# Optimization experiments

Hardware: AMD Instinct MI355X
Metric: run time of the kernel (lower is better)

Reference implementation:

```python
import jax, jax.numpy as jnp
import numpy as np

V, N, K, D = 2, 100000, 8, 128
TAU = 1.0
LOG_2PI = float(np.log(2.0 * np.pi))


def setup_inputs() -> dict:
    key = jax.random.key(0)
    k1, k2, k3 = jax.random.split(key, 3)
    z = jax.random.normal(k1, (V, N, D), dtype=jnp.float32)
    phi = jnp.ones((V, K), dtype=jnp.float32) / K
    mu = jax.random.normal(k2, (V, K, D), dtype=jnp.float32)
    # sigma: identity (as in torch init) plus a small symmetric PSD perturbation
    a = 0.05 * jax.random.normal(k3, (V, K, D, D), dtype=jnp.float32)
    sigma = jnp.eye(D, dtype=jnp.float32) + jnp.einsum('vkde,vkfe->vkdf', a, a)
    return {"z": z, "phi": phi, "mu": mu, "sigma": sigma}


def _compute_energy(z, phi, mu, sigma):
    # z: [N, D]; phi: [K]; mu: [K, D]; sigma: [K, D, D]
    eps_eye = 1e-6 * jnp.eye(D, dtype=z.dtype)
    sigma_stable = sigma + eps_eye  # [K, D, D]
    inv_sigma = jnp.linalg.inv(sigma_stable)
    det_sigma = jnp.clip(jnp.linalg.det(sigma_stable), 1e-6, None)  # [K]
    diff = z[:, None, :] - mu[None, :, :]  # [N, K, D]
    maha = jnp.einsum('nkd,kde,nke->nk', diff, inv_sigma, diff)  # [N, K]
    log_pi = jax.nn.log_softmax(phi)  # [K]
    log_prob = (-0.5 * maha
                - 0.5 * D * LOG_2PI
                - 0.5 * jnp.log(det_sigma)[None, :]
                + log_pi[None, :])  # [N, K]
    energy = -jax.nn.logsumexp(log_prob, axis=1)  # [N]
    penalty = jnp.sum(1.0 / (jnp.diagonal(sigma_stable, axis1=-2, axis2=-1) + 1e-12))
    return energy, penalty


def reference(z, phi, mu, sigma):
    # vmap over views; energies_v: [V, N]
    energies_v, penalties = jax.vmap(_compute_energy)(z, phi, mu, sigma)
    energies = energies_v.T  # [N, V]
    total_energies = jnp.sum(energies)
    total_penalty = jnp.sum(penalties)
    weights = jax.nn.softmax(-energies / TAU, axis=1)  # [N, V]
    return energies, weights, total_energies, total_penalty
```

## Files before the change

kernel.cpp:

```cpp
#include <hip/hip_runtime.h>
#include <math.h>

#define V 2
#define NN 100000
#define KK 8
#define DD 128
#define TILE_N 128
#define SL 132
#define NT 782
#define CH 8
#define NCHUNK 98
#define NPAD 100096
#define LOG2PI 1.8378770664093454f
#define LOG_1EM6 -13.815510557964274f

#define IMG_B 69632
#define IMG_HALF 17408
#define LF_B   1114112
#define BV_B   2228224
#define C_B    2236416
#define MAHA_B 2236480

#define OUT_W_OFF (NN*V)
#define OUT_TE (2*NN*V)
#define OUT_TP (2*NN*V + 1)

typedef __attribute__((ext_vector_type(8))) short bf16x8;
typedef __attribute__((ext_vector_type(4))) float f32x4;
typedef __attribute__((ext_vector_type(4))) unsigned u32x4;

__device__ __forceinline__ unsigned short f2bf_rtn(float f) {
    unsigned u = __builtin_bit_cast(unsigned, f);
    unsigned r = u + 0x7FFFu + ((u >> 16) & 1u);
    return (unsigned short)(r >> 16);
}
__device__ __forceinline__ float bf2f(unsigned short h) {
    unsigned u = ((unsigned)h) << 16;
    return __builtin_bit_cast(float, u);
}

__device__ __forceinline__ void cvt_pair(float f0, float f1, unsigned& hi, unsigned& lo) {
    unsigned u0 = __builtin_bit_cast(unsigned, f0);
    unsigned u1 = __builtin_bit_cast(unsigned, f1);
    hi = __builtin_amdgcn_perm(u1, u0, 0x07060302u);
    float r0 = f0 - __builtin_bit_cast(float, u0 & 0xFFFF0000u);
    float r1 = f1 - __builtin_bit_cast(float, u1 & 0xFFFF0000u);
    unsigned v0 = __builtin_bit_cast(unsigned, r0) + 0x8000u;
    unsigned v1 = __builtin_bit_cast(unsigned, r1) + 0x8000u;
    lo = __builtin_amdgcn_perm(v1, v0, 0x07060302u);
}

__global__ void zero_kernel(float* out) {
    int t = threadIdx.x;
    if (t < 2) out[OUT_TE + t] = 0.0f;
}

__global__ __launch_bounds__(256) void prep_chol(const float* __restrict__ phi,
                                                 const float* __restrict__ mu,
                                                 const float* __restrict__ sigma,
                                                 void* __restrict__ wsv,
                                                 float* __restrict__ out) {
    __shared__ float Lf[DD * SL];
    __shared__ float P[8][SL];
    __shared__ float dvec[DD];
    __shared__ float mulds[DD];
    __shared__ float red[256];
    __shared__ float Bv[8];
    __shared__ float Bb[DD];

    const int tid = threadIdx.x;
    const int vk  = blockIdx.x;
    const int v   = vk >> 3;
    const int k   = vk & 7;
    const int R   = tid >> 4;
    const int C   = tid & 15;

    if (tid < DD) mulds[tid] = mu[vk * DD + tid];

    float A[8][8];
    const float* sig = sigma + (size_t)vk * DD * DD;
    float pen = 0.0f;
    #pragma unroll
    for (int a = 0; a < 8; ++a) {
        const float4* p4 = (const float4*)(sig + (size_t)(8 * R + a) * DD + 8 * C);
        float4 x = p4[0], y = p4[1];
        A[a][0] = x.x; A[a][1] = x.y; A[a][2] = x.z; A[a][3] = x.w;
        A[a][4] = y.x; A[a][5] = y.y; A[a][6] = y.z; A[a][7] = y.w;
        if (R == C) A[a][a] += 1e-6f;
    }
    if (R == C) {
        #pragma unroll
        for (int a = 0; a < 8; ++a) pen += 1.0f / (A[a][a] + 1e-12f);
    }

    for (int i = tid; i < DD * SL; i += 256) Lf[i] = 0.0f;

    red[tid] = pen;
    __syncthreads();
    for (int s = 128; s > 0; s >>= 1) {
        if (tid < s) red[tid] += red[tid + s];
        __syncthreads();
    }
    if (tid == 0) atomicAdd(&out[OUT_TP], red[0]);
    __syncthreads();

    for (int p = 0; p < 16; ++p) {
        if (C == p && R >= p) {
            #pragma unroll
            for (int b = 0; b < 8; ++b) {
                *(float4*)&P[b][8 * R]     = make_float4(A[0][b], A[1][b], A[2][b], A[3][b]);
                *(float4*)&P[b][8 * R + 4] = make_float4(A[4][b], A[5][b], A[6][b], A[7][b]);
            }
        }
        __syncthreads();

        if (tid < 64) {
            const int lane = tid;
            const int r1 = 8 * p + lane;
            const int r2 = r1 + 64;
            const bool ok2 = (r2 < DD);
            float pr1[8], pr2[8], rs[8];
            #pragma unroll
            for (int j = 0; j < 8; ++j) {
                pr1[j] = (r1 < DD) ? P[j][r1] : 0.0f;
                pr2[j] = ok2 ? P[j][r2] : 0.0f;
            }
            #pragma unroll
            for (int j = 0; j < 8; ++j) {
                if (lane >= j && lane < 8) Bv[lane] = pr1[j];
                __builtin_amdgcn_wave_barrier();
                float bv[8];
                #pragma unroll
                for (int m = 0; m < 8; ++m) bv[m] = Bv[m];
                __builtin_amdgcn_wave_barrier();
                float piv = bv[j];
                if (lane == j) dvec[8 * p + j] = piv;
                float inv2 = 1.0f / piv;
                rs[j] = rsqrtf(piv);
                float m1 = pr1[j] * inv2;
                float m2 = pr2[j] * inv2;
                #pragma unroll
                for (int j2 = 0; j2 < 8; ++j2) {
                    if (j2 > j) {
                        if (lane > j) pr1[j2] -= m1 * bv[j2];
                        pr2[j2] -= m2 * bv[j2];
                    }
                }
            }
            #pragma unroll
            for (int j = 0; j < 8; ++j) {
                if (r1 < DD) {
                    float v1 = (lane >= j) ? pr1[j] * rs[j] : 0.0f;
                    P[j][r1] = v1;
                    Lf[r1 * SL + 8 * p + j] = v1;
                }
                if (ok2) {
                    float v2 = pr2[j] * rs[j];
                    P[j][r2] = v2;
                    Lf[r2 * SL + 8 * p + j] = v2;
                }
            }
        }
        __syncthreads();

        if (C > p && R >= p) {
            #pragma unroll
            for (int j = 0; j < 8; ++j) {
                float4 a0 = *(const float4*)&P[j][8 * R];
                float4 a1 = *(const float4*)&P[j][8 * R + 4];
                float4 b0 = *(const float4*)&P[j][8 * C];
                float4 b1 = *(const float4*)&P[j][8 * C + 4];
                float ra[8] = {a0.x, a0.y, a0.z, a0.w, a1.x, a1.y, a1.z, a1.w};
                float rb[8] = {b0.x, b0.y, b0.z, b0.w, b1.x, b1.y, b1.z, b1.w};
                #pragma unroll
                for (int a = 0; a < 8; ++a)
                    #pragma unroll
                    for (int b = 0; b < 8; ++b)
                        A[a][b] -= ra[a] * rb[b];
            }
        }
        __syncthreads();
    }

    if (tid < 64) {
        const int lane = tid;
        float acc0 = mulds[lane];
        float acc1 = mulds[lane + 64];
        for (int j = 0; j < DD; ++j) {
            if (j < 64) { if (lane == j)      Bb[j] = acc0 / Lf[j * SL + j]; }
            else        { if (lane == j - 64) Bb[j] = acc1 / Lf[j * SL + j]; }
            __builtin_amdgcn_wave_barrier();
            float bj = Bb[j];
            __builtin_amdgcn_wave_barrier();
            if (lane > j)      acc0 -= Lf[lane * SL + j] * bj;
            if (lane + 64 > j) acc1 -= Lf[(lane + 64) * SL + j] * bj;
        }
    }
    __syncthreads();
    if (tid < DD) ((float*)((char*)wsv + BV_B))[vk * DD + tid] = Bb[tid];

    {
        float4* Lg = (float4*)((char*)wsv + LF_B + (size_t)vk * IMG_B);
        const float4* Ls4 = (const float4*)Lf;
        for (int i = tid; i < DD * SL / 4; i += 256) Lg[i] = Ls4[i];
    }

    red[tid] = (tid < DD) ? logf(dvec[tid]) : 0.0f;
    __syncthreads();
    for (int s = 128; s > 0; s >>= 1) {
        if (tid < s) red[tid] += red[tid + s];
        __syncthreads();
    }
    if (tid == 0) {
        float logdet_c = fmaxf(red[0], LOG_1EM6);
        const float* ph = phi + v * KK;
        float m = ph[0];
        for (int i = 1; i < KK; ++i) m = fmaxf(m, ph[i]);
        float s = 0.0f;
        for (int i = 0; i < KK; ++i) s += expf(ph[i] - m);
        float logpi = ph[k] - m - logf(s);
        ((float*)((char*)wsv + C_B))[vk] = logpi - 0.5f * logdet_c - 0.5f * (float)DD * LOG2PI;
    }
}

__global__ __launch_bounds__(256) void prep_trsm(void* __restrict__ wsv) {
    __shared__ float Ls[DD * SL];
    __shared__ float Wc[32][SL];

    const int tid = threadIdx.x;
    const int vk  = blockIdx.x >> 2;
    const int cg  = blockIdx.x & 3;

    const float4* Lg = (const float4*)((const char*)wsv + LF_B + (size_t)vk * IMG_B);
    float4* Ls4 = (float4*)Ls;
    for (int i = tid; i < DD * SL / 4; i += 256) Ls4[i] = Lg[i];
    __syncthreads();

    const int c   = tid >> 3;
    const int par = tid & 7;
    const int j   = 4 * c + cg;

    for (int e = par; e < SL; e += 8) Wc[c][e] = 0.0f;
    if (par == 0) Wc[c][j] = 1.0f / Ls[j * SL + j];
    __builtin_amdgcn_wave_barrier();

    const int pbase = j & ~3;
    for (int i = j + 1; i < DD; ++i) {
        float s = 0.0f;
        for (int p4 = pbase + 4 * par; p4 < i; p4 += 32) {
            float4 lf = *(const float4*)&Ls[i * SL + p4];
            float4 wc = *(const float4*)&Wc[c][p4];
            s += lf.x * wc.x + lf.y * wc.y + lf.z * wc.z + lf.w * wc.w;
        }
        s += __shfl_xor(s, 1, 64);
        s += __shfl_xor(s, 2, 64);
        s += __shfl_xor(s, 4, 64);
        if (par == 0) Wc[c][i] = -s / Ls[i * SL + i];
        __builtin_amdgcn_wave_barrier();
    }

    unsigned short* Gh = (unsigned short*)((char*)wsv + (size_t)vk * IMG_B);
    unsigned short* Gl = Gh + IMG_HALF;
    for (int i2 = par; i2 < DD; i2 += 8) {
        float f = (i2 >= j) ? Wc[c][i2] : 0.0f;
        unsigned short h = f2bf_rtn(f);
        unsigned short l = f2bf_rtn(f - bf2f(h));
        Gh[i2 * 136 + j] = h;
        Gl[i2 * 136 + j] = l;
    }
}

__global__ __launch_bounds__(256, 2) void maha_kernel(const float* __restrict__ z,
                                                      void* __restrict__ wsv) {
    __shared__ unsigned short wl[IMG_B / 2];
    __shared__ float bl_s[DD];

    const int tid  = threadIdx.x;
    const int lane = tid & 63;
    const int wave = tid >> 6;
    const int quad = lane >> 4;
    const int l16  = lane & 15;
    const int r     = blockIdx.x;
    const int chunk = blockIdx.y;
    const int vv    = r >> 3;

    {
        const char* src = (const char*)wsv + (size_t)r * IMG_B;
        char* dst = (char*)wl;
        const int lane_off = wave * 1024 + lane * 16;
        #pragma unroll
        for (int t = 0; t < 17; ++t)
            __builtin_amdgcn_global_load_lds(
                (const __attribute__((address_space(1))) void*)(src + t * 4096 + lane_off),
                (__attribute__((address_space(3))) void*)(dst + t * 4096 + wave * 1024),
                16, 0, 0);
    }
    if (tid < DD) bl_s[tid] = ((const float*)((const char*)wsv + BV_B))[r * DD + tid];
    __syncthreads();

    const float* zbase = z + (size_t)vv * NN * DD;
    float* mrow = (float*)((char*)wsv + MAHA_B) + (size_t)r * NPAD;

    for (int ti = 0; ti < CH; ++ti) {
        const int t = chunk * CH + ti;
        if (t >= NT) break;
        const int n0 = t * TILE_N;

        f32x4 acc[2][8];
        #pragma unroll
        for (int mt = 0; mt < 2; ++mt)
            #pragma unroll
            for (int nt = 0; nt < 8; ++nt)
                acc[mt][nt] = (f32x4)(0.0f);

        #pragma unroll
        for (int ds = 0; ds < 4; ++ds) {
            u32x4 zh[2], zl[2];
            #pragma unroll
            for (int mt = 0; mt < 2; ++mt) {
                const int n = n0 + wave * 32 + mt * 16 + l16;
                float f[8];
                if (n < NN) {
                    const float* zp = zbase + (size_t)n * DD + quad * 8 + ds * 32;
                    float4 a  = *(const float4*)(zp);
                    float4 bq = *(const float4*)(zp + 4);
                    f[0] = a.x;  f[1] = a.y;  f[2] = a.z;  f[3] = a.w;
                    f[4] = bq.x; f[5] = bq.y; f[6] = bq.z; f[7] = bq.w;
                } else {
                    #pragma unroll
                    for (int e = 0; e < 8; ++e) f[e] = 0.0f;
                }
                #pragma unroll
                for (int d = 0; d < 4; ++d) {
                    unsigned hi, lo;
                    cvt_pair(f[2 * d], f[2 * d + 1], hi, lo);
                    zh[mt][d] = hi;
                    zl[mt][d] = lo;
                }
            }

            const int g = ds * 4 + quad;
            #pragma unroll
            for (int nt = 2 * ds; nt < 8; ++nt) {
                const int row = nt * 16 + l16;
                const int off = row * 136 + g * 8;
                bf16x8 bh  = *(const bf16x8*)&wl[off];
                bf16x8 blo = *(const bf16x8*)&wl[IMG_HALF + off];
                #pragma unroll
                for (int mt = 0; mt < 2; ++mt) {
                    bf16x8 ah = __builtin_bit_cast(bf16x8, zh[mt]);
                    bf16x8 al = __builtin_bit_cast(bf16x8, zl[mt]);
                    acc[mt][nt] = __builtin_amdgcn_mfma_f32_16x16x32_bf16(ah, bh,  acc[mt][nt], 0, 0, 0);
                    acc[mt][nt] = __builtin_amdgcn_mfma_f32_16x16x32_bf16(ah, blo, acc[mt][nt], 0, 0, 0);
                    acc[mt][nt] = __builtin_amdgcn_mfma_f32_16x16x32_bf16(al, bh,  acc[mt][nt], 0, 0, 0);
                }
            }
        }

        #pragma unroll
        for (int mt = 0; mt < 2; ++mt) {
            float p[4] = {0.f, 0.f, 0.f, 0.f};
            #pragma unroll
            for (int nt = 0; nt < 8; ++nt) {
                float bc = bl_s[nt * 16 + l16];
                f32x4 a = acc[mt][nt];
                float y0 = a[0] - bc, y1 = a[1] - bc, y2 = a[2] - bc, y3 = a[3] - bc;
                p[0] += y0 * y0; p[1] += y1 * y1; p[2] += y2 * y2; p[3] += y3 * y3;
            }
            float sv[4];
            #pragma unroll
            for (int reg = 0; reg < 4; ++reg) {
                float s = p[reg];
                s += __shfl_xor(s, 1, 64);
                s += __shfl_xor(s, 2, 64);
                s += __shfl_xor(s, 4, 64);
                s += __shfl_xor(s, 8, 64);
                sv[reg] = s;
            }
            if (l16 == 0)
                *(float4*)&mrow[n0 + wave * 32 + mt * 16 + quad * 4] =
                    make_float4(sv[0], sv[1], sv[2], sv[3]);
        }
    }
}

__global__ __launch_bounds__(256) void finalize_kernel(const void* __restrict__ wsv,
                                                       float* __restrict__ out) {
    __shared__ float red[256];
    __shared__ float clds[16];

    const int tid = threadIdx.x;
    if (tid < 16) clds[tid] = ((const float*)((const char*)wsv + C_B))[tid];
    __syncthreads();

    const float* mahap = (const float*)((const char*)wsv + MAHA_B);
    const int n = blockIdx.x * 256 + tid;
    float esum = 0.0f;

    if (n < NN) {
        float ev[V];
        #pragma unroll
        for (int vv = 0; vv < V; ++vv) {
            float lp[KK];
            float m = -1e30f;
            #pragma unroll
            for (int k = 0; k < KK; ++k) {
                int r = vv * KK + k;
                lp[k] = -0.5f * mahap[(size_t)r * NPAD + n] + clds[r];
                m = fmaxf(m, lp[k]);
            }
            float s = 0.0f;
            #pragma unroll
            for (int k = 0; k < KK; ++k) s += expf(lp[k] - m);
            ev[vv] = -(m + logf(s));
        }
        float e0 = ev[0], e1 = ev[1];
        float m = fmaxf(-e0, -e1);
        float x0 = expf(-e0 - m);
        float x1 = expf(-e1 - m);
        float inv = 1.0f / (x0 + x1);
        out[(size_t)n * V + 0] = e0;
        out[(size_t)n * V + 1] = e1;
        out[OUT_W_OFF + (size_t)n * V + 0] = x0 * inv;
        out[OUT_W_OFF + (size_t)n * V + 1] = x1 * inv;
        esum = e0 + e1;
    }

    red[tid] = esum;
    __syncthreads();
    for (int s = 128; s > 0; s >>= 1) {
        if (tid < s) red[tid] += red[tid + s];
        __syncthreads();
    }
    if (tid == 0) atomicAdd(&out[OUT_TE], red[0]);
}

extern "C" void kernel_launch(void* const* d_in, const int* in_sizes, int n_in,
                              void* d_out, int out_size, void* d_ws, size_t ws_size,
                              hipStream_t stream) {
    const float* z     = (const float*)d_in[0];
    const float* phi   = (const float*)d_in[1];
    const float* mu    = (const float*)d_in[2];
    const float* sigma = (const float*)d_in[3];
    float* out = (float*)d_out;

    hipLaunchKernelGGL(zero_kernel, dim3(1), dim3(64), 0, stream, out);
    hipLaunchKernelGGL(prep_chol, dim3(V * KK), dim3(256), 0, stream, phi, mu, sigma, d_ws, out);
    hipLaunchKernelGGL(prep_trsm, dim3(64), dim3(256), 0, stream, d_ws);
    hipLaunchKernelGGL(maha_kernel, dim3(16, NCHUNK), dim3(256), 0, stream, z, d_ws);
    hipLaunchKernelGGL(finalize_kernel, dim3((NPAD + 255) / 256), dim3(256), 0, stream, d_ws, out);
}
```

Measured before the change: 427.8 us.

## Prefetch next z tile into registers and remap blocks for XCD locality

The maha kernel now loads the whole next tile of z into registers while the MFMA work for the current tile runs, so global load latency is hidden behind compute. The launch grid is flattened and remapped so that all 16 (view, component) blocks sharing a chunk of z land on the same XCD, which should improve L2 reuse of z. Blocks whose chunk falls past the end of the data exit early. The change raises register pressure from the prefetch buffers and the full zh/zl arrays, which could lower occupancy under launch_bounds(256,2).

Measured after the change: 393.6 us. 8.0% less time.

```diff
diff --git a/kernel.cpp b/kernel.cpp
--- a/kernel.cpp
+++ b/kernel.cpp
@@ -9,7 +9,7 @@
 #define SL 132
 #define NT 782
 #define CH 8
-#define NCHUNK 98
+#define CPX 13
 #define NPAD 100096
 #define LOG2PI 1.8378770664093454f
 #define LOG_1EM6 -13.815510557964274f
@@ -280,9 +280,16 @@
     const int wave = tid >> 6;
     const int quad = lane >> 4;
     const int l16  = lane & 15;
-    const int r     = blockIdx.x;
-    const int chunk = blockIdx.y;
+
+    const int bi    = blockIdx.x;
+    const int xcd   = bi & 7;
+    const int jj    = bi >> 3;
+    const int r     = jj & 15;
+    const int lc    = jj >> 4;
+    const int chunk = xcd * CPX + lc;
     const int vv    = r >> 3;
+
+    if (chunk * CH >= NT) return;
 
     {
         const char* src = (const char*)wsv + (size_t)r * IMG_B;
@@ -301,11 +308,55 @@
     const float* zbase = z + (size_t)vv * NN * DD;
     float* mrow = (float*)((char*)wsv + MAHA_B) + (size_t)r * NPAD;
 
+    float4 pre[2][4][2];
+
+    auto load_tile = [&](int tt) {
+        #pragma unroll
+        for (int mt = 0; mt < 2; ++mt) {
+            const int n = tt * TILE_N + wave * 32 + mt * 16 + l16;
+            const bool ok = (n < NN);
+            const float* zp = zbase + (size_t)n * DD + quad * 8;
+            #pragma unroll
+            for (int ds = 0; ds < 4; ++ds) {
+                if (ok) {
+                    pre[mt][ds][0] = *(const float4*)(zp + ds * 32);
+                    pre[mt][ds][1] = *(const float4*)(zp + ds * 32 + 4);
+                } else {
+                    pre[mt][ds][0] = make_float4(0.f, 0.f, 0.f, 0.f);
+                    pre[mt][ds][1] = make_float4(0.f, 0.f, 0.f, 0.f);
+                }
+            }
+        }
+    };
+
+    load_tile(chunk * CH);
+
     for (int ti = 0; ti < CH; ++ti) {
         const int t = chunk * CH + ti;
         if (t >= NT) break;
         const int n0 = t * TILE_N;
 
+        u32x4 zh[2][4], zl[2][4];
+        #pragma unroll
+        for (int mt = 0; mt < 2; ++mt)
+            #pragma unroll
+            for (int ds = 0; ds < 4; ++ds) {
+                float4 a = pre[mt][ds][0];
+                float4 b = pre[mt][ds][1];
+                unsigned h0, l0, h1, l1, h2, l2, h3, l3;
+                cvt_pair(a.x, a.y, h0, l0);
+                cvt_pair(a.z, a.w, h1, l1);
+                cvt_pair(b.x, b.y, h2, l2);
+                cvt_pair(b.z, b.w, h3, l3);
+                u32x4 th, tl;
+                th[0] = h0; th[1] = h1; th[2] = h2; th[3] = h3;
+                tl[0] = l0; tl[1] = l1; tl[2] = l2; tl[3] = l3;
+                zh[mt][ds] = th;
+                zl[mt][ds] = tl;
+            }
+
+        if (ti + 1 < CH && t + 1 < NT) load_tile(t + 1);
+
         f32x4 acc[2][8];
         #pragma unroll
         for (int mt = 0; mt < 2; ++mt)
@@ -315,30 +366,6 @@
 
         #pragma unroll
         for (int ds = 0; ds < 4; ++ds) {
-            u32x4 zh[2], zl[2];
-            #pragma unroll
-            for (int mt = 0; mt < 2; ++mt) {
-                const int n = n0 + wave * 32 + mt * 16 + l16;
-                float f[8];
-                if (n < NN) {
-                    const float* zp = zbase + (size_t)n * DD + quad * 8 + ds * 32;
-                    float4 a  = *(const float4*)(zp);
-                    float4 bq = *(const float4*)(zp + 4);
-                    f[0] = a.x;  f[1] = a.y;  f[2] = a.z;  f[3] = a.w;
-                    f[4] = bq.x; f[5] = bq.y; f[6] = bq.z; f[7] = bq.w;
-                } else {
-                    #pragma unroll
-                    for (int e = 0; e < 8; ++e) f[e] = 0.0f;
-                }
-                #pragma unroll
-                for (int d = 0; d < 4; ++d) {
-                    unsigned hi, lo;
-                    cvt_pair(f[2 * d], f[2 * d + 1], hi, lo);
-                    zh[mt][d] = hi;
-                    zl[mt][d] = lo;
-                }
-            }
-
             const int g = ds * 4 + quad;
             #pragma unroll
             for (int nt = 2 * ds; nt < 8; ++nt) {
@@ -348,8 +375,8 @@
                 bf16x8 blo = *(const bf16x8*)&wl[IMG_HALF + off];
                 #pragma unroll
                 for (int mt = 0; mt < 2; ++mt) {
-                    bf16x8 ah = __builtin_bit_cast(bf16x8, zh[mt]);
-                    bf16x8 al = __builtin_bit_cast(bf16x8, zl[mt]);
+                    bf16x8 ah = __builtin_bit_cast(bf16x8, zh[mt][ds]);
+                    bf16x8 al = __builtin_bit_cast(bf16x8, zl[mt][ds]);
                     acc[mt][nt] = __builtin_amdgcn_mfma_f32_16x16x32_bf16(ah, bh,  acc[mt][nt], 0, 0, 0);
                     acc[mt][nt] = __builtin_amdgcn_mfma_f32_16x16x32_bf16(ah, blo, acc[mt][nt], 0, 0, 0);
                     acc[mt][nt] = __builtin_amdgcn_mfma_f32_16x16x32_bf16(al, bh,  acc[mt][nt], 0, 0, 0);
@@ -447,6 +474,6 @@
     hipLaunchKernelGGL(zero_kernel, dim3(1), dim3(64), 0, stream, out);
     hipLaunchKernelGGL(prep_chol, dim3(V * KK), dim3(256), 0, stream, phi, mu, sigma, d_ws, out);
     hipLaunchKernelGGL(prep_trsm, dim3(64), dim3(256), 0, stream, d_ws);
-    hipLaunchKernelGGL(maha_kernel, dim3(16, NCHUNK), dim3(256), 0, stream, z, d_ws);
+    hipLaunchKernelGGL(maha_kernel, dim3(8 * CPX * 16), dim3(256), 0, stream, z, d_ws);
     hipLaunchKernelGGL(finalize_kernel, dim3((NPAD + 255) / 256), dim3(256), 0, stream, d_ws, out);
 }
```
